# Kernel tuning notes

Hardware: AMD Instinct MI355X
Metric: run time of the kernel (lower is better)

The kernel has to match this reference:

```python
import jax, jax.numpy as jnp
import numpy as np

B, S, D = 4, 2048, 1024


def setup_inputs() -> dict:
    key = jax.random.key(0)
    kq, k1, k2, k3 = jax.random.split(key, 4)
    w_scale = 1.0 / np.sqrt(D)  # ~ glorot scale for square Dense
    q = jax.random.normal(kq, (B, S, D), dtype=jnp.float32)
    Wq = jax.random.normal(k1, (D, D), dtype=jnp.float32) * w_scale
    Wk = jax.random.normal(k2, (D, D), dtype=jnp.float32) * w_scale  # unused in self-attn path (bug in original)
    Wv = jax.random.normal(k3, (D, D), dtype=jnp.float32) * w_scale
    # causal mask: 1 = masked (future), matching tf.where(mask == 1, -1e9, scores)
    mask = jnp.triu(jnp.ones((S, S), dtype=jnp.int32), k=1)
    return {"q": q, "Wq": Wq, "Wk": Wk, "Wv": Wv, "mask": mask}


def reference(q, Wq, Wk, Wv, mask):
    # Self-attention path of the original: k=None, v=None.
    WQ = jnp.einsum('bsd,de->bse', q, Wq)
    # Faithful to the original code: dense_v is applied for BOTH K and V.
    WKV = jnp.einsum('bsd,de->bse', q, Wv)
    d_k = jnp.asarray(D, dtype=q.dtype)
    scores = jnp.einsum('bqd,bkd->bqk', WQ, WKV) / jnp.sqrt(d_k)  # [B,S,S]
    scores = jnp.where(mask == 1, jnp.asarray(-1e9, scores.dtype), scores)
    attn = jax.nn.softmax(scores, axis=-1)
    return jnp.einsum('bqk,bkd->bqd', attn, WKV)
```

## Files before the change

kernel.cpp:

```cpp
#include <hip/hip_runtime.h>


typedef unsigned short u16;
typedef short short8 __attribute__((ext_vector_type(8)));
typedef float floatx4 __attribute__((ext_vector_type(4)));

#define S_LEN 2048
#define D_DIM 1024
#define BK 64

__device__ inline u16 f2b(float f) {
  unsigned u = __float_as_uint(f);
  return (u16)((u + 0x7fffu + ((u >> 16) & 1u)) >> 16);
}

__device__ __forceinline__ void gload16(const u16* g, u16* l) {
  __builtin_amdgcn_global_load_lds(
      (const __attribute__((address_space(1))) void*)g,
      (__attribute__((address_space(3))) void*)l, 16, 0, 0);
}

__global__ __launch_bounds__(256)
void cvt_f32_bf16(const float* __restrict__ src, u16* __restrict__ dst) {
  size_t idx = ((size_t)blockIdx.x * 256 + threadIdx.x) * 8;
  float4 a0 = *(const float4*)&src[idx];
  float4 a1 = *(const float4*)&src[idx + 4];
  short8 v;
  v[0] = (short)f2b(a0.x); v[1] = (short)f2b(a0.y);
  v[2] = (short)f2b(a0.z); v[3] = (short)f2b(a0.w);
  v[4] = (short)f2b(a1.x); v[5] = (short)f2b(a1.y);
  v[6] = (short)f2b(a1.z); v[7] = (short)f2b(a1.w);
  *(short8*)&dst[idx] = v;
}

__global__ __launch_bounds__(256)
void transpose_cvt2(const float* __restrict__ s0, u16* __restrict__ d0_,
                    const float* __restrict__ s1, u16* __restrict__ d1_) {
  __shared__ u16 tile[32][33];
  const float* src = blockIdx.z ? s1 : s0;
  u16* dst = blockIdx.z ? d1_ : d0_;
  int c0 = blockIdx.x * 32, r0 = blockIdx.y * 32;
  int tx = threadIdx.x, ty = threadIdx.y;
  for (int ii = 0; ii < 32; ii += 8)
    tile[ii + ty][tx] = f2b(src[(size_t)(r0 + ii + ty) * 1024 + (c0 + tx)]);
  __syncthreads();
  for (int ii = 0; ii < 32; ii += 8)
    dst[(size_t)(c0 + ii + ty) * 1024 + (r0 + tx)] = tile[tx][ii + ty];
}

__global__ __launch_bounds__(256)
void transpose_bf16(const u16* __restrict__ src, u16* __restrict__ dst, int R, int C) {
  __shared__ u16 tile[32][33];
  size_t bo = (size_t)blockIdx.z * R * C;
  const u16* s = src + bo;
  u16* d = dst + bo;
  int c0 = blockIdx.x * 32, r0 = blockIdx.y * 32;
  int tx = threadIdx.x, ty = threadIdx.y;
  for (int ii = 0; ii < 32; ii += 8)
    tile[ii + ty][tx] = s[(size_t)(r0 + ii + ty) * C + (c0 + tx)];
  __syncthreads();
  for (int ii = 0; ii < 32; ii += 8)
    d[(size_t)(c0 + ii + ty) * R + (r0 + tx)] = tile[tx][ii + ty];
}

#define GEMM_PROLOG()                                                         \
  __shared__ u16 Als[128 * BK];                                               \
  __shared__ u16 Bls[128 * BK];                                               \
  int tid = threadIdx.x;                                                      \
  int wave = tid >> 6, lane = tid & 63, quad = lane >> 4, l15 = lane & 15;    \
  int wm = (wave >> 1) * 64, wn = (wave & 1) * 64;                            \
  int arow = lane >> 3;                                                       \
  int acol = ((lane & 7) ^ (arow & 7)) << 3;                                  \
  floatx4 acc[4][4];                                                          \
  _Pragma("unroll") for (int i = 0; i < 4; ++i)                               \
  _Pragma("unroll") for (int j = 0; j < 4; ++j)                               \
      acc[i][j] = (floatx4){0.f, 0.f, 0.f, 0.f};

#define GEMM_KLOOP(Aptr, lda, Bptr, ldb, KEND)                                \
  for (int kb = 0; kb < (KEND); kb += BK) {                                   \
    __syncthreads();                                                          \
    _Pragma("unroll") for (int p = 0; p < 4; ++p) {                           \
      int r0 = p * 32 + wave * 8;                                             \
      gload16(&(Aptr)[(size_t)(m0 + r0 + arow) * (lda) + kb + acol],          \
              &Als[r0 * BK]);                                                 \
      gload16(&(Bptr)[(size_t)(n0 + r0 + arow) * (ldb) + kb + acol],          \
              &Bls[r0 * BK]);                                                 \
    }                                                                         \
    __syncthreads();                                                          \
    _Pragma("unroll") for (int kk8 = 0; kk8 < 8; kk8 += 4) {                  \
      int cg = (((kk8 + quad) & 7) ^ (l15 & 7)) << 3;                         \
      short8 af[4], bfr[4];                                                   \
      _Pragma("unroll") for (int i = 0; i < 4; ++i)                           \
          af[i] = *(const short8*)&Als[(wm + i * 16 + l15) * BK + cg];        \
      _Pragma("unroll") for (int j = 0; j < 4; ++j)                           \
          bfr[j] = *(const short8*)&Bls[(wn + j * 16 + l15) * BK + cg];       \
      _Pragma("unroll") for (int i = 0; i < 4; ++i)                           \
      _Pragma("unroll") for (int j = 0; j < 4; ++j)                           \
          acc[i][j] = __builtin_amdgcn_mfma_f32_16x16x32_bf16(                \
              af[i], bfr[j], acc[i][j], 0, 0, 0);                             \
    }                                                                         \
  }

#define GEMM64_PROLOG()                                                       \
  __shared__ u16 Als[64 * BK];                                                \
  __shared__ u16 Bls[128 * BK];                                               \
  int tid = threadIdx.x;                                                      \
  int wave = tid >> 6, lane = tid & 63, quad = lane >> 4, l15 = lane & 15;    \
  int wr = (wave >> 1) * 32, wc = (wave & 1) * 64;                            \
  int arow = lane >> 3;                                                       \
  int acol = ((lane & 7) ^ (arow & 7)) << 3;                                  \
  floatx4 acc[2][4];                                                          \
  _Pragma("unroll") for (int i = 0; i < 2; ++i)                               \
  _Pragma("unroll") for (int j = 0; j < 4; ++j)                               \
      acc[i][j] = (floatx4){0.f, 0.f, 0.f, 0.f};

#define GEMM64_KLOOP(Aptr, lda, Bptr, ldb, KEND)                              \
  for (int kb = 0; kb < (KEND); kb += BK) {                                   \
    __syncthreads();                                                          \
    _Pragma("unroll") for (int p = 0; p < 2; ++p) {                           \
      int r0 = wave * 16 + p * 8;                                             \
      gload16(&(Aptr)[(size_t)(m0 + r0 + arow) * (lda) + kb + acol],          \
              &Als[r0 * BK]);                                                 \
    }                                                                         \
    _Pragma("unroll") for (int p = 0; p < 4; ++p) {                           \
      int r0 = wave * 32 + p * 8;                                             \
      gload16(&(Bptr)[(size_t)(n0 + r0 + arow) * (ldb) + kb + acol],          \
              &Bls[r0 * BK]);                                                 \
    }                                                                         \
    __syncthreads();                                                          \
    _Pragma("unroll") for (int kk8 = 0; kk8 < 8; kk8 += 4) {                  \
      int cg = (((kk8 + quad) & 7) ^ (l15 & 7)) << 3;                         \
      short8 af[2], bfr[4];                                                   \
      _Pragma("unroll") for (int i = 0; i < 2; ++i)                           \
          af[i] = *(const short8*)&Als[(wr + i * 16 + l15) * BK + cg];        \
      _Pragma("unroll") for (int j = 0; j < 4; ++j)                           \
          bfr[j] = *(const short8*)&Bls[(wc + j * 16 + l15) * BK + cg];       \
      _Pragma("unroll") for (int i = 0; i < 2; ++i)                           \
      _Pragma("unroll") for (int j = 0; j < 4; ++j)                           \
          acc[i][j] = __builtin_amdgcn_mfma_f32_16x16x32_bf16(                \
              af[i], bfr[j], acc[i][j], 0, 0, 0);                             \
    }                                                                         \
  }

__global__ __launch_bounds__(256)
void gemm_proj(const u16* __restrict__ A, const u16* __restrict__ B0,
               const u16* __restrict__ B1, u16* __restrict__ C0,
               u16* __restrict__ C1) {
  int m0 = blockIdx.y * 128, n0 = blockIdx.x * 128;
  const u16* Bp = blockIdx.z ? B1 : B0;
  u16* Cp = blockIdx.z ? C1 : C0;
  GEMM_PROLOG();
  GEMM_KLOOP(A, D_DIM, Bp, D_DIM, D_DIM);
#pragma unroll
  for (int i = 0; i < 4; ++i)
#pragma unroll
    for (int j = 0; j < 4; ++j)
#pragma unroll
      for (int r = 0; r < 4; ++r)
        Cp[(size_t)(m0 + wm + i * 16 + quad * 4 + r) * D_DIM +
           (n0 + wn + j * 16 + l15)] = f2b(acc[i][j][r]);
}

__global__ __launch_bounds__(256)
void gemm_scores(const u16* __restrict__ WQ, const u16* __restrict__ WKV,
                 u16* __restrict__ Pp, float* __restrict__ rowsum) {
  int id = blockIdx.x;
  int x = id & 7;
  int b = x & 3;
  int t = (id >> 3) * 2 + (x >> 2);
  int m = (int)((sqrtf(4.f * (float)t + 1.f) - 1.f) * 0.5f);
  while ((m + 1) * (m + 2) <= t) ++m;
  while (m * (m + 1) > t) --m;
  int rem = t - m * (m + 1);
  int bi = (rem < m + 1) ? 2 * m : 2 * m + 1;
  int bj = (rem < m + 1) ? rem : rem - (m + 1);
  int m0 = bi * 64, n0 = bj * 128;
  const u16* A = WQ + (size_t)b * S_LEN * D_DIM;
  const u16* Bp = WKV + (size_t)b * S_LEN * D_DIM;
  GEMM64_PROLOG();
  GEMM64_KLOOP(A, D_DIM, Bp, D_DIM, D_DIM);
  u16* Pb = Pp + (size_t)b * S_LEN * S_LEN;
  float part[2][4];
#pragma unroll
  for (int i = 0; i < 2; ++i)
#pragma unroll
    for (int r = 0; r < 4; ++r) part[i][r] = 0.f;
#pragma unroll
  for (int i = 0; i < 2; ++i)
#pragma unroll
    for (int j = 0; j < 4; ++j) {
      int col = n0 + wc + j * 16 + l15;
#pragma unroll
      for (int r = 0; r < 4; ++r) {
        int row = m0 + wr + i * 16 + quad * 4 + r;
        float p = (col > row) ? 0.f : __expf(acc[i][j][r] * 0.03125f);
        Pb[(size_t)row * S_LEN + col] = f2b(p);
        part[i][r] += p;
      }
    }
#pragma unroll
  for (int i = 0; i < 2; ++i)
#pragma unroll
    for (int r = 0; r < 4; ++r) {
      float v = part[i][r];
#pragma unroll
      for (int off = 1; off < 16; off <<= 1) v += __shfl_xor(v, off, 64);
      part[i][r] = v;
    }
  if (l15 == 0) {
#pragma unroll
    for (int i = 0; i < 2; ++i)
#pragma unroll
      for (int r = 0; r < 4; ++r)
        atomicAdd(&rowsum[b * S_LEN + m0 + wr + i * 16 + quad * 4 + r],
                  part[i][r]);
  }
}

__global__ __launch_bounds__(256)
void gemm_pv(const u16* __restrict__ Pp, const u16* __restrict__ WKVt,
             const float* __restrict__ rowsum, float* __restrict__ out) {
  int id = blockIdx.x;
  int x = id & 7;
  int b = x & 3;
  int r_ = (id >> 3) * 2 + (x >> 2);
  int bi = 31 - (r_ >> 3), bj = r_ & 7;
  int m0 = bi * 64, n0 = bj * 128;
  int kend = (bi + 1) * 64;
  const u16* A = Pp + (size_t)b * S_LEN * S_LEN;
  const u16* Bp = WKVt + (size_t)b * (size_t)D_DIM * S_LEN;
  GEMM64_PROLOG();
  GEMM64_KLOOP(A, S_LEN, Bp, S_LEN, kend);
  const float* rs = rowsum + b * S_LEN;
  float* Co = out + (size_t)b * S_LEN * D_DIM;
#pragma unroll
  for (int i = 0; i < 2; ++i)
#pragma unroll
    for (int r = 0; r < 4; ++r) {
      int row = m0 + wr + i * 16 + quad * 4 + r;
      float inv = 1.0f / rs[row];
#pragma unroll
      for (int j = 0; j < 4; ++j)
        Co[(size_t)row * D_DIM + (n0 + wc + j * 16 + l15)] =
            acc[i][j][r] * inv;
    }
}

extern "C" void kernel_launch(void* const* d_in, const int* in_sizes, int n_in,
                              void* d_out, int out_size, void* d_ws, size_t ws_size,
                              hipStream_t stream) {
  const float* q = (const float*)d_in[0];
  const float* Wq = (const float*)d_in[1];
  const float* Wv = (const float*)d_in[3];
  char* ws = (char*)d_ws;
  const size_t MB = 1024 * 1024;
  u16* Wqt = (u16*)(ws);
  u16* Wvt = (u16*)(ws + 2 * MB);
  u16* qb16 = (u16*)(ws + 4 * MB);
  u16* Pp = (u16*)(ws);
  u16* WQ = (u16*)(ws + 32 * MB);
  u16* WKV = (u16*)(ws + 48 * MB);
  u16* WKVt = (u16*)(ws + 64 * MB);
  float* rowsum = (float*)(ws + 80 * MB);

  hipMemsetAsync(rowsum, 0, 4 * S_LEN * sizeof(float), stream);
  cvt_f32_bf16<<<4096, 256, 0, stream>>>(q, qb16);
  transpose_cvt2<<<dim3(32, 32, 2), dim3(32, 8), 0, stream>>>(Wq, Wqt, Wv, Wvt);
  gemm_proj<<<dim3(8, 64, 2), 256, 0, stream>>>(qb16, Wqt, Wvt, WQ, WKV);
  transpose_bf16<<<dim3(32, 64, 4), dim3(32, 8), 0, stream>>>(WKV, WKVt, 2048, 1024);
  gemm_scores<<<1088, 256, 0, stream>>>(WQ, WKV, Pp, rowsum);
  gemm_pv<<<1024, 256, 0, stream>>>(Pp, WKVt, rowsum, (float*)d_out);
}
```

Before: 230.2 us.

## Fuse WKV transpose into projection GEMM epilogue and remap blocks for XCD locality

The projection GEMM now writes the transposed WKV tile through shared memory in its epilogue, which removes the separate transpose kernel launch and its extra global read/write pass. All three GEMMs switch to a 1D grid whose block-to-tile mapping keeps each batch, and the rows that share operands, on the same XCD so L2 reuse improves. The cost is a larger shared buffer and extra epilogue work in the V-projection blocks.

```diff
diff --git a/kernel.cpp b/kernel.cpp
--- a/kernel.cpp
+++ b/kernel.cpp
@@ -49,57 +49,88 @@
 }
 
 __global__ __launch_bounds__(256)
-void transpose_bf16(const u16* __restrict__ src, u16* __restrict__ dst, int R, int C) {
-  __shared__ u16 tile[32][33];
-  size_t bo = (size_t)blockIdx.z * R * C;
-  const u16* s = src + bo;
-  u16* d = dst + bo;
-  int c0 = blockIdx.x * 32, r0 = blockIdx.y * 32;
-  int tx = threadIdx.x, ty = threadIdx.y;
-  for (int ii = 0; ii < 32; ii += 8)
-    tile[ii + ty][tx] = s[(size_t)(r0 + ii + ty) * C + (c0 + tx)];
-  __syncthreads();
-  for (int ii = 0; ii < 32; ii += 8)
-    d[(size_t)(c0 + ii + ty) * R + (r0 + tx)] = tile[tx][ii + ty];
-}
-
-#define GEMM_PROLOG()                                                         \
-  __shared__ u16 Als[128 * BK];                                               \
-  __shared__ u16 Bls[128 * BK];                                               \
-  int tid = threadIdx.x;                                                      \
-  int wave = tid >> 6, lane = tid & 63, quad = lane >> 4, l15 = lane & 15;    \
-  int wm = (wave >> 1) * 64, wn = (wave & 1) * 64;                            \
-  int arow = lane >> 3;                                                       \
-  int acol = ((lane & 7) ^ (arow & 7)) << 3;                                  \
-  floatx4 acc[4][4];                                                          \
-  _Pragma("unroll") for (int i = 0; i < 4; ++i)                               \
-  _Pragma("unroll") for (int j = 0; j < 4; ++j)                               \
-      acc[i][j] = (floatx4){0.f, 0.f, 0.f, 0.f};
-
-#define GEMM_KLOOP(Aptr, lda, Bptr, ldb, KEND)                                \
-  for (int kb = 0; kb < (KEND); kb += BK) {                                   \
-    __syncthreads();                                                          \
-    _Pragma("unroll") for (int p = 0; p < 4; ++p) {                           \
-      int r0 = p * 32 + wave * 8;                                             \
-      gload16(&(Aptr)[(size_t)(m0 + r0 + arow) * (lda) + kb + acol],          \
-              &Als[r0 * BK]);                                                 \
-      gload16(&(Bptr)[(size_t)(n0 + r0 + arow) * (ldb) + kb + acol],          \
-              &Bls[r0 * BK]);                                                 \
-    }                                                                         \
-    __syncthreads();                                                          \
-    _Pragma("unroll") for (int kk8 = 0; kk8 < 8; kk8 += 4) {                  \
-      int cg = (((kk8 + quad) & 7) ^ (l15 & 7)) << 3;                         \
-      short8 af[4], bfr[4];                                                   \
-      _Pragma("unroll") for (int i = 0; i < 4; ++i)                           \
-          af[i] = *(const short8*)&Als[(wm + i * 16 + l15) * BK + cg];        \
-      _Pragma("unroll") for (int j = 0; j < 4; ++j)                           \
-          bfr[j] = *(const short8*)&Bls[(wn + j * 16 + l15) * BK + cg];       \
-      _Pragma("unroll") for (int i = 0; i < 4; ++i)                           \
-      _Pragma("unroll") for (int j = 0; j < 4; ++j)                           \
-          acc[i][j] = __builtin_amdgcn_mfma_f32_16x16x32_bf16(                \
-              af[i], bfr[j], acc[i][j], 0, 0, 0);                             \
-    }                                                                         \
-  }
+void gemm_proj(const u16* __restrict__ A, const u16* __restrict__ B0,
+               const u16* __restrict__ B1, u16* __restrict__ C0,
+               u16* __restrict__ C1, u16* __restrict__ WKVt) {
+  int id = blockIdx.x;
+  int xcd = id & 7, i = id >> 3;
+  int m_idx = xcd * 8 + (i & 7);
+  int nz = i >> 3;
+  int n0 = (nz & 7) * 128, z = nz >> 3;
+  int m0 = m_idx * 128;
+  const u16* Bp = z ? B1 : B0;
+  u16* Cp = z ? C1 : C0;
+  __shared__ __align__(16) char smem[34816];
+  u16* Als = (u16*)smem;
+  u16* Bls = (u16*)(smem + 16384);
+  u16* Tls = (u16*)smem;
+  int tid = threadIdx.x;
+  int wave = tid >> 6, lane = tid & 63, quad = lane >> 4, l15 = lane & 15;
+  int wm = (wave >> 1) * 64, wn = (wave & 1) * 64;
+  int arow = lane >> 3;
+  int acol = ((lane & 7) ^ (arow & 7)) << 3;
+  floatx4 acc[4][4];
+#pragma unroll
+  for (int ii = 0; ii < 4; ++ii)
+#pragma unroll
+    for (int j = 0; j < 4; ++j) acc[ii][j] = (floatx4){0.f, 0.f, 0.f, 0.f};
+  for (int kb = 0; kb < D_DIM; kb += BK) {
+    __syncthreads();
+#pragma unroll
+    for (int p = 0; p < 4; ++p) {
+      int r0 = p * 32 + wave * 8;
+      gload16(&A[(size_t)(m0 + r0 + arow) * D_DIM + kb + acol], &Als[r0 * BK]);
+      gload16(&Bp[(size_t)(n0 + r0 + arow) * D_DIM + kb + acol], &Bls[r0 * BK]);
+    }
+    __syncthreads();
+#pragma unroll
+    for (int kk8 = 0; kk8 < 8; kk8 += 4) {
+      int cg = (((kk8 + quad) & 7) ^ (l15 & 7)) << 3;
+      short8 af[4], bfr[4];
+#pragma unroll
+      for (int ii = 0; ii < 4; ++ii)
+        af[ii] = *(const short8*)&Als[(wm + ii * 16 + l15) * BK + cg];
+#pragma unroll
+      for (int j = 0; j < 4; ++j)
+        bfr[j] = *(const short8*)&Bls[(wn + j * 16 + l15) * BK + cg];
+#pragma unroll
+      for (int ii = 0; ii < 4; ++ii)
+#pragma unroll
+        for (int j = 0; j < 4; ++j)
+          acc[ii][j] = __builtin_amdgcn_mfma_f32_16x16x32_bf16(
+              af[ii], bfr[j], acc[ii][j], 0, 0, 0);
+    }
+  }
+#pragma unroll
+  for (int ii = 0; ii < 4; ++ii)
+#pragma unroll
+    for (int j = 0; j < 4; ++j)
+#pragma unroll
+      for (int r = 0; r < 4; ++r)
+        Cp[(size_t)(m0 + wm + ii * 16 + quad * 4 + r) * D_DIM +
+           (n0 + wn + j * 16 + l15)] = f2b(acc[ii][j][r]);
+  if (z) {
+    __syncthreads();
+#pragma unroll
+    for (int ii = 0; ii < 4; ++ii)
+#pragma unroll
+      for (int j = 0; j < 4; ++j)
+#pragma unroll
+        for (int r = 0; r < 4; ++r)
+          Tls[(wn + j * 16 + l15) * 136 + (wm + ii * 16 + quad * 4 + r)] =
+              f2b(acc[ii][j][r]);
+    __syncthreads();
+    int b = m0 >> 11, srow = m0 & 2047;
+    u16* Wt = WKVt + (size_t)b * D_DIM * S_LEN;
+#pragma unroll
+    for (int p = 0; p < 8; ++p) {
+      int e = p * 2048 + tid * 8;
+      int d = e >> 7, s = e & 127;
+      *(short8*)&Wt[(size_t)(n0 + d) * S_LEN + srow + s] =
+          *(const short8*)&Tls[d * 136 + s];
+    }
+  }
+}
 
 #define GEMM64_PROLOG()                                                       \
   __shared__ u16 Als[64 * BK];                                                \
@@ -143,37 +174,17 @@
   }
 
 __global__ __launch_bounds__(256)
-void gemm_proj(const u16* __restrict__ A, const u16* __restrict__ B0,
-               const u16* __restrict__ B1, u16* __restrict__ C0,
-               u16* __restrict__ C1) {
-  int m0 = blockIdx.y * 128, n0 = blockIdx.x * 128;
-  const u16* Bp = blockIdx.z ? B1 : B0;
-  u16* Cp = blockIdx.z ? C1 : C0;
-  GEMM_PROLOG();
-  GEMM_KLOOP(A, D_DIM, Bp, D_DIM, D_DIM);
-#pragma unroll
-  for (int i = 0; i < 4; ++i)
-#pragma unroll
-    for (int j = 0; j < 4; ++j)
-#pragma unroll
-      for (int r = 0; r < 4; ++r)
-        Cp[(size_t)(m0 + wm + i * 16 + quad * 4 + r) * D_DIM +
-           (n0 + wn + j * 16 + l15)] = f2b(acc[i][j][r]);
-}
-
-__global__ __launch_bounds__(256)
 void gemm_scores(const u16* __restrict__ WQ, const u16* __restrict__ WKV,
                  u16* __restrict__ Pp, float* __restrict__ rowsum) {
   int id = blockIdx.x;
-  int x = id & 7;
-  int b = x & 3;
-  int t = (id >> 3) * 2 + (x >> 2);
-  int m = (int)((sqrtf(4.f * (float)t + 1.f) - 1.f) * 0.5f);
-  while ((m + 1) * (m + 2) <= t) ++m;
-  while (m * (m + 1) > t) --m;
-  int rem = t - m * (m + 1);
-  int bi = (rem < m + 1) ? 2 * m : 2 * m + 1;
-  int bj = (rem < m + 1) ? rem : rem - (m + 1);
+  int xcd = id & 7;
+  int b = xcd & 3, h = xcd >> 2;
+  int t = id >> 3;
+  int m = (int)((sqrtf(8.f * (float)t + 1.f) - 1.f) * 0.5f);
+  while ((m + 1) * (m + 2) / 2 <= t) ++m;
+  while (m * (m + 1) / 2 > t) --m;
+  int bj = t - m * (m + 1) / 2;
+  int bi = 2 * m + h;
   int m0 = bi * 64, n0 = bj * 128;
   const u16* A = WQ + (size_t)b * S_LEN * D_DIM;
   const u16* Bp = WKV + (size_t)b * S_LEN * D_DIM;
@@ -221,10 +232,12 @@
 void gemm_pv(const u16* __restrict__ Pp, const u16* __restrict__ WKVt,
              const float* __restrict__ rowsum, float* __restrict__ out) {
   int id = blockIdx.x;
-  int x = id & 7;
-  int b = x & 3;
-  int r_ = (id >> 3) * 2 + (x >> 2);
-  int bi = 31 - (r_ >> 3), bj = r_ & 7;
+  int xcd = id & 7;
+  int b = xcd & 3, h = xcd >> 2;
+  int r_ = id >> 3;
+  int mh = 15 - (r_ >> 3);
+  int bi = 2 * mh + h;
+  int bj = r_ & 7;
   int m0 = bi * 64, n0 = bj * 128;
   int kend = (bi + 1) * 64;
   const u16* A = Pp + (size_t)b * S_LEN * S_LEN;
@@ -266,8 +279,7 @@
   hipMemsetAsync(rowsum, 0, 4 * S_LEN * sizeof(float), stream);
   cvt_f32_bf16<<<4096, 256, 0, stream>>>(q, qb16);
   transpose_cvt2<<<dim3(32, 32, 2), dim3(32, 8), 0, stream>>>(Wq, Wqt, Wv, Wvt);
-  gemm_proj<<<dim3(8, 64, 2), 256, 0, stream>>>(qb16, Wqt, Wvt, WQ, WKV);
-  transpose_bf16<<<dim3(32, 64, 4), dim3(32, 8), 0, stream>>>(WKV, WKVt, 2048, 1024);
+  gemm_proj<<<1024, 256, 0, stream>>>(qb16, Wqt, Wvt, WQ, WKV, WKVt);
   gemm_scores<<<1088, 256, 0, stream>>>(WQ, WKV, Pp, rowsum);
   gemm_pv<<<1024, 256, 0, stream>>>(Pp, WKVt, rowsum, (float*)d_out);
 }
```

Measured after the change: 213.2 us. 7.4% less time.
